# Optimization experiments

Measured on AMD Instinct MI355X. Metric: run time of the kernel, lower is better.

## Reference

```python
import jax, jax.numpy as jnp
import numpy as np

N = 2_000_000
N_IN = 128
N_HID = 32
CT_SIZE = 16384  # n_bags(1024) * n_ct(16)
N_CT = 16


def setup_inputs() -> dict:
    key = jax.random.key(0)
    ks = jax.random.split(key, 10)
    X = jax.random.normal(ks[0], (N, N_IN), dtype=jnp.float32)
    batch = jax.random.randint(ks[1], (N,), 0, CT_SIZE, dtype=jnp.int32)
    s = 1.0 / np.sqrt(N_IN)
    W1 = jax.random.uniform(ks[2], (N_IN, N_HID), jnp.float32, -s, s)
    b1 = jax.random.uniform(ks[3], (N_HID,), jnp.float32, -s, s)
    s2 = 1.0 / np.sqrt(N_HID)
    wc = jax.random.uniform(ks[4], (N_HID, 1), jnp.float32, -s2, s2)
    bc = jax.random.uniform(ks[5], (1,), jnp.float32, -s2, s2)
    wct = jax.random.uniform(ks[6], (N_HID, 1), jnp.float32, -s2, s2)
    bct = jax.random.uniform(ks[7], (1,), jnp.float32, -s2, s2)
    Wout = jax.random.uniform(ks[8], (N_HID, 1), jnp.float32, -s2, s2)
    bout = jax.random.uniform(ks[9], (1,), jnp.float32, -s2, s2)
    return {"X": X, "W1": W1, "b1": b1, "wc": wc, "bc": bc,
            "wct": wct, "bct": bct, "Wout": Wout, "bout": bout,
            "batch": batch, "ct_size": CT_SIZE, "n_ct": N_CT}


def _segment_softmax(s, batch, num_segments):
    # numerically stable softmax within each segment
    m = jax.ops.segment_max(s, batch, num_segments=num_segments)
    e = jnp.exp(s - m[batch])
    denom = jax.ops.segment_sum(e, batch, num_segments=num_segments)
    return e / denom[batch]


def reference(X, W1, b1, wc, bc, wct, bct, Wout, bout, batch, ct_size, n_ct):
    # lin: Linear(n_in, n_hid) + ReLU (dropout=0 in eval)
    H = jax.nn.relu(X @ W1 + b1)                          # [N, n_hid]
    # attn1 with use_softmax: segment softmax over cells within each (bag, celltype) segment
    s = (H @ wc + bc)[:, 0]                               # [N]
    w_c = _segment_softmax(s, batch, ct_size)             # [N]
    # global_add_pool of attention-weighted features, reshape to [n_bags, n_ct, n_hid]
    P = jax.ops.segment_sum(H * w_c[:, None], batch, num_segments=ct_size)
    P = P.reshape(-1, n_ct, N_HID)                        # [B, n_ct, n_hid]
    # lin2 is empty (n_layers_lin2=0)
    # attn2: softmax over cell-type axis
    w_ct = jax.nn.softmax(P @ wct + bct, axis=1)          # [B, n_ct, 1]
    Xb = jnp.sum(P * w_ct, axis=1)                        # [B, n_hid]
    return Xb @ Wout + bout                               # [B, 1]
```

## Files before the change

### kernel.cpp

```cpp
#include <hip/hip_runtime.h>
#include <hip/hip_bf16.h>
#include <cmath>

#define NIN   128
#define NHID  32
#define CTS   16384
#define NCT   16
#define NBAGS (CTS / NCT)
#define CAP   256
#define NBLK  128
#define SEG_STRIDE 33

typedef __attribute__((ext_vector_type(8))) short bf16x8;
typedef __attribute__((ext_vector_type(4))) float f32x4;

__device__ inline ushort f2bf(float f) {
    uint x = __float_as_uint(f);
    uint r = (x + 0x7fffu + ((x >> 16) & 1u)) >> 16;
    return (ushort)r;
}
__device__ inline float bf2f(ushort b) { return __uint_as_float(((uint)b) << 16); }


__global__ __launch_bounds__(1024) void hist_kernel(
    const int* __restrict__ batch, uint* __restrict__ hist, int n, int chunk)
{
    __shared__ uint h[CTS];
    const int b = blockIdx.x;
    for (int i = threadIdx.x; i < CTS; i += 1024) h[i] = 0;
    __syncthreads();
    const int lo = b * chunk, hi = min(n, lo + chunk);
    for (int i = lo + threadIdx.x; i < hi; i += 1024)
        atomicAdd(&h[batch[i]], 1u);
    __syncthreads();
    uint* __restrict__ hb = hist + (size_t)b * CTS;
    for (int i = threadIdx.x; i < CTS; i += 1024) hb[i] = h[i];
}

__global__ __launch_bounds__(256) void prefix_kernel(
    uint* __restrict__ hist, int* __restrict__ cnt)
{
    const int s = blockIdx.x * 256 + threadIdx.x;
    if (s >= CTS) return;
    uint run = 0;
#pragma unroll 4
    for (int b = 0; b < NBLK; ++b) {
        const uint t = hist[(size_t)b * CTS + s];
        hist[(size_t)b * CTS + s] = run;
        run += t;
    }
    cnt[s * 16] = (int)run;
}

__global__ __launch_bounds__(1024) void place_kernel(
    const int* __restrict__ batch, const uint* __restrict__ hist,
    int* __restrict__ slots, int n, int chunk)
{
    __shared__ uint h[CTS];
    const int b = blockIdx.x;
    const uint* __restrict__ hb = hist + (size_t)b * CTS;
    for (int i = threadIdx.x; i < CTS; i += 1024) h[i] = hb[i];
    __syncthreads();
    const int lo = b * chunk, hi = min(n, lo + chunk);
    for (int i = lo + threadIdx.x; i < hi; i += 1024) {
        const int s = batch[i];
        const uint pos = atomicAdd(&h[s], 1u);
        if (pos < CAP) slots[(size_t)s * CAP + pos] = i;
    }
}

__global__ __launch_bounds__(256) void seg_kernel(
    const float* __restrict__ X,
    const float* __restrict__ W1,
    const float* __restrict__ b1,
    const float* __restrict__ wc,
    const float* __restrict__ bc,
    const int*   __restrict__ cnt,
    const int*   __restrict__ slots,
    float* __restrict__ P)
{
    __shared__ __align__(16) float w1s[NIN * NHID];

    const int tid = threadIdx.x;
    for (int i = tid; i < NIN * NHID / 4; i += 256)
        ((float4*)w1s)[i] = ((const float4*)W1)[i];
    __syncthreads();

    const int w    = tid >> 6;
    const int lane = tid & 63;
    const int g    = lane >> 4;
    const int c    = lane & 15;
    const int s    = blockIdx.x * 4 + w;
    const int m    = min(cnt[s * 16], CAP);

    bf16x8 Bh[4][2], Bl[4][2];
#pragma unroll
    for (int kc = 0; kc < 4; ++kc) {
#pragma unroll
        for (int nh = 0; nh < 2; ++nh) {
            union { bf16x8 v; ushort u[8]; } bh, bl;
#pragma unroll
            for (int e = 0; e < 8; ++e) {
                const float wv = w1s[(kc * 32 + g * 8 + e) * NHID + nh * 16 + c];
                const ushort h = f2bf(wv);
                bh.u[e] = h;
                bl.u[e] = f2bf(wv - bf2f(h));
            }
            Bh[kc][nh] = bh.v;
            Bl[kc][nh] = bl.v;
        }
    }

    const float b1c0 = b1[c], b1c1 = b1[c + 16];
    const float wc0  = wc[c], wc1  = wc[c + 16];
    const float bc0  = bc[0];

    float pacc0 = 0.f, pacc1 = 0.f, esum = 0.f;
    const int ntiles = (m + 15) >> 4;
    const size_t sbase = (size_t)s * CAP;

    auto slot_of = [&](int t) -> int {
        const int ti = t * 16 + c;
        return slots[sbase + min(ti, m - 1)];
    };

    auto compute_tile = [&](const float4* x, int t) {
        f32x4 acc0 = {0.f, 0.f, 0.f, 0.f};
        f32x4 acc1 = {0.f, 0.f, 0.f, 0.f};
#pragma unroll
        for (int kc = 0; kc < 4; ++kc) {
            const float xs[8] = {x[2*kc].x, x[2*kc].y, x[2*kc].z, x[2*kc].w,
                                 x[2*kc+1].x, x[2*kc+1].y, x[2*kc+1].z, x[2*kc+1].w};
            union { bf16x8 v; __hip_bfloat162 h2[4]; } ah;
#pragma unroll
            for (int e = 0; e < 4; ++e)
                ah.h2[e] = __float22bfloat162_rn(make_float2(xs[2*e], xs[2*e+1]));

            acc0 = __builtin_amdgcn_mfma_f32_16x16x32_bf16(ah.v, Bh[kc][0], acc0, 0, 0, 0);
            acc0 = __builtin_amdgcn_mfma_f32_16x16x32_bf16(ah.v, Bl[kc][0], acc0, 0, 0, 0);
            acc1 = __builtin_amdgcn_mfma_f32_16x16x32_bf16(ah.v, Bh[kc][1], acc1, 0, 0, 0);
            acc1 = __builtin_amdgcn_mfma_f32_16x16x32_bf16(ah.v, Bl[kc][1], acc1, 0, 0, 0);
        }
#pragma unroll
        for (int i = 0; i < 4; ++i) {
            const float h0 = fmaxf(acc0[i] + b1c0, 0.f);
            const float h1 = fmaxf(acc1[i] + b1c1, 0.f);
            float sp = h0 * wc0 + h1 * wc1;
            sp += __shfl_xor(sp, 1);
            sp += __shfl_xor(sp, 2);
            sp += __shfl_xor(sp, 4);
            sp += __shfl_xor(sp, 8);
            const int row = t * 16 + g * 4 + i;
            const float e = (row < m) ? expf(sp + bc0) : 0.f;
            pacc0 = fmaf(e, h0, pacc0);
            pacc1 = fmaf(e, h1, pacc1);
            esum += e;
        }
    };

    auto load_tile = [&](float4* x, int r) {
        const float4* __restrict__ xr = (const float4*)(X + (size_t)r * NIN);
#pragma unroll
        for (int kc = 0; kc < 4; ++kc) {
            x[2*kc]   = xr[kc * 8 + g * 2];
            x[2*kc+1] = xr[kc * 8 + g * 2 + 1];
        }
    };

    if (ntiles > 0) {
        float4 xa[8];
        load_tile(xa, slot_of(0));
        int rnext = (ntiles > 1) ? slot_of(1) : 0;

        for (int t = 0; t < ntiles; ++t) {
            float4 xb[8];
            const bool more = (t + 1) < ntiles;
            if (more) load_tile(xb, rnext);
            const int rnn = (t + 2 < ntiles) ? slot_of(t + 2) : 0;
            compute_tile(xa, t);
#pragma unroll
            for (int q = 0; q < 8; ++q) xa[q] = xb[q];
            rnext = rnn;
        }
    }

    pacc0 += __shfl_xor(pacc0, 16); pacc0 += __shfl_xor(pacc0, 32);
    pacc1 += __shfl_xor(pacc1, 16); pacc1 += __shfl_xor(pacc1, 32);
    esum  += __shfl_xor(esum, 16);  esum  += __shfl_xor(esum, 32);

    if (lane < 16) {
        const float inv = esum > 0.f ? 1.f / esum : 0.f;
        P[(size_t)s * NHID + c]      = pacc0 * inv;
        P[(size_t)s * NHID + 16 + c] = pacc1 * inv;
    }
}

__global__ __launch_bounds__(256) void bags_kernel(
    const float* __restrict__ P,
    const float* __restrict__ wct,
    const float* __restrict__ bct,
    const float* __restrict__ Wout,
    const float* __restrict__ bout,
    float* __restrict__ out)
{
    const int b = blockIdx.x * blockDim.x + threadIdx.x;
    if (b >= NBAGS) return;

    float logit[NCT], dout[NCT];
#pragma unroll
    for (int ct = 0; ct < NCT; ++ct) {
        const float* p = P + (size_t)(b * NCT + ct) * NHID;
        float t = 0.f, d = 0.f;
#pragma unroll
        for (int j = 0; j < NHID; ++j) {
            const float pj = p[j];
            t += pj * wct[j];
            d += pj * Wout[j];
        }
        logit[ct] = t + bct[0];
        dout[ct]  = d;
    }

    float mx = logit[0];
#pragma unroll
    for (int ct = 1; ct < NCT; ++ct) mx = fmaxf(mx, logit[ct]);
    float den = 0.f, accv = 0.f;
#pragma unroll
    for (int ct = 0; ct < NCT; ++ct) {
        const float e = expf(logit[ct] - mx);
        den += e;
        accv += e * dout[ct];
    }
    out[b] = accv / den + bout[0];
}


__global__ __launch_bounds__(256) void rows_kernel_atomic(
    const float* __restrict__ X, const float* __restrict__ W1,
    const float* __restrict__ b1, const float* __restrict__ wc,
    const float* __restrict__ bc, const int* __restrict__ batch,
    float* __restrict__ segacc, int n)
{
    const long long r0 = (long long)blockIdx.x * 256 + threadIdx.x;
    if (r0 >= n) return;
    const float4* xp = (const float4*)(X + (size_t)r0 * NIN);
    float acc[NHID];
#pragma unroll
    for (int j = 0; j < NHID; ++j) acc[j] = 0.f;
#pragma unroll 4
    for (int kc = 0; kc < NIN / 4; ++kc) {
        const float4 xv = xp[kc];
        const float xa[4] = {xv.x, xv.y, xv.z, xv.w};
#pragma unroll
        for (int kk = 0; kk < 4; ++kk) {
            const float* wrow = W1 + (kc * 4 + kk) * NHID;
            const float u = xa[kk];
#pragma unroll
            for (int j = 0; j < NHID; ++j) acc[j] = fmaf(u, wrow[j], acc[j]);
        }
    }
    float sc = bc[0];
#pragma unroll
    for (int j = 0; j < NHID; ++j) {
        const float h = fmaxf(acc[j] + b1[j], 0.f); acc[j] = h; sc += h * wc[j];
    }
    const float e = expf(sc);
    float* p = segacc + (size_t)batch[r0] * SEG_STRIDE;
#pragma unroll
    for (int j = 0; j < NHID; ++j) atomicAdd(p + j, e * acc[j]);
    atomicAdd(p + NHID, e);
}

__global__ __launch_bounds__(256) void bags_kernel_fb(
    const float* __restrict__ segacc, const float* __restrict__ wct,
    const float* __restrict__ bct, const float* __restrict__ Wout,
    const float* __restrict__ bout, float* __restrict__ out)
{
    const int b = blockIdx.x * blockDim.x + threadIdx.x;
    if (b >= NBAGS) return;
    float logit[NCT], dout[NCT];
#pragma unroll
    for (int ct = 0; ct < NCT; ++ct) {
        const float* p = segacc + (size_t)(b * NCT + ct) * SEG_STRIDE;
        const float den = p[NHID];
        const float inv = den > 0.f ? 1.f / den : 0.f;
        float t = 0.f, d = 0.f;
#pragma unroll
        for (int j = 0; j < NHID; ++j) { const float pj = p[j]*inv; t += pj*wct[j]; d += pj*Wout[j]; }
        logit[ct] = t + bct[0];
        dout[ct]  = d;
    }
    float mx = logit[0];
#pragma unroll
    for (int ct = 1; ct < NCT; ++ct) mx = fmaxf(mx, logit[ct]);
    float den = 0.f, accv = 0.f;
#pragma unroll
    for (int ct = 0; ct < NCT; ++ct) {
        const float e = expf(logit[ct] - mx);
        den += e; accv += e * dout[ct];
    }
    out[b] = accv / den + bout[0];
}


extern "C" void kernel_launch(void* const* d_in, const int* in_sizes, int n_in,
                              void* d_out, int out_size, void* d_ws, size_t ws_size,
                              hipStream_t stream)
{
    const float* X    = (const float*)d_in[0];
    const float* W1   = (const float*)d_in[1];
    const float* b1   = (const float*)d_in[2];
    const float* wc   = (const float*)d_in[3];
    const float* bc   = (const float*)d_in[4];
    const float* wct  = (const float*)d_in[5];
    const float* bct  = (const float*)d_in[6];
    const float* Wout = (const float*)d_in[7];
    const float* bout = (const float*)d_in[8];
    const int*   batch= (const int*)d_in[9];
    const int n = in_sizes[9];

    const size_t cnt_bytes  = (size_t)CTS * 16 * sizeof(int);
    const size_t slot_bytes = (size_t)CTS * CAP * sizeof(int);
    const size_t p_bytes    = (size_t)CTS * NHID * sizeof(float);
    const size_t hist_bytes = (size_t)NBLK * CTS * sizeof(uint);
    const size_t need = cnt_bytes + slot_bytes + p_bytes + hist_bytes;

    if (ws_size >= need) {
        int*   cnt   = (int*)d_ws;
        int*   slots = cnt + (size_t)CTS * 16;
        float* P     = (float*)(slots + (size_t)CTS * CAP);
        uint*  hist  = (uint*)(P + (size_t)CTS * NHID);

        const int chunk = (n + NBLK - 1) / NBLK;
        hist_kernel<<<NBLK, 1024, 0, stream>>>(batch, hist, n, chunk);
        prefix_kernel<<<CTS / 256, 256, 0, stream>>>(hist, cnt);
        place_kernel<<<NBLK, 1024, 0, stream>>>(batch, hist, slots, n, chunk);
        seg_kernel<<<CTS / 4, 256, 0, stream>>>(X, W1, b1, wc, bc, cnt, slots, P);
        bags_kernel<<<(NBAGS + 255) / 256, 256, 0, stream>>>(
            P, wct, bct, Wout, bout, (float*)d_out);
    } else {
        float* segacc = (float*)d_ws;
        hipMemsetAsync(segacc, 0, (size_t)CTS * SEG_STRIDE * sizeof(float), stream);
        rows_kernel_atomic<<<(n + 255) / 256, 256, 0, stream>>>(
            X, W1, b1, wc, bc, batch, segacc, n);
        bags_kernel_fb<<<(NBAGS + 255) / 256, 256, 0, stream>>>(
            segacc, wct, bct, Wout, bout, (float*)d_out);
    }
}
```

Baseline: 310.1 us.

## Process three segments per wave with interleaved tile loads; double histogram blocks

Each wave in the segment kernel now handles three segments, round-robin interleaving their tiles so the X-row loads for one segment overlap the MFMA compute of the others. The goal is more memory-level parallelism and amortising the per-block W1 split-bf16 setup over more segments. Separately, the histogram and placement kernels use twice as many blocks. In exchange, register pressure rises from the three tile buffers and the grid gets fewer blocks, which may lower occupancy. The histogram workspace also doubles.

```diff
diff --git a/kernel.cpp b/kernel.cpp
--- a/kernel.cpp
+++ b/kernel.cpp
@@ -8,7 +8,7 @@
 #define NCT   16
 #define NBAGS (CTS / NCT)
 #define CAP   256
-#define NBLK  128
+#define NBLK  256
 #define SEG_STRIDE 33
 
 typedef __attribute__((ext_vector_type(8))) short bf16x8;
@@ -90,8 +90,6 @@
     const int lane = tid & 63;
     const int g    = lane >> 4;
     const int c    = lane & 15;
-    const int s    = blockIdx.x * 4 + w;
-    const int m    = min(cnt[s * 16], CAP);
 
     bf16x8 Bh[4][2], Bl[4][2];
 #pragma unroll
@@ -115,16 +113,33 @@
     const float wc0  = wc[c], wc1  = wc[c + 16];
     const float bc0  = bc[0];
 
-    float pacc0 = 0.f, pacc1 = 0.f, esum = 0.f;
-    const int ntiles = (m + 15) >> 4;
-    const size_t sbase = (size_t)s * CAP;
-
-    auto slot_of = [&](int t) -> int {
-        const int ti = t * 16 + c;
-        return slots[sbase + min(ti, m - 1)];
+    const int sBase = blockIdx.x * 12 + w * 3;
+    const int s0 = sBase, s1 = sBase + 1, s2 = sBase + 2;
+    const bool v0 = s0 < CTS, v1 = s1 < CTS, v2 = s2 < CTS;
+    const int m0 = v0 ? min(cnt[s0 * 16], CAP) : 0;
+    const int m1 = v1 ? min(cnt[s1 * 16], CAP) : 0;
+    const int m2 = v2 ? min(cnt[s2 * 16], CAP) : 0;
+    const int n0 = (m0 + 15) >> 4, n1 = (m1 + 15) >> 4, n2 = (m2 + 15) >> 4;
+
+    float pa00 = 0.f, pa01 = 0.f, es0 = 0.f;
+    float pa10 = 0.f, pa11 = 0.f, es1 = 0.f;
+    float pa20 = 0.f, pa21 = 0.f, es2 = 0.f;
+
+    auto slot_of = [&](int s, int m, int t) -> int {
+        return slots[(size_t)s * CAP + min(t * 16 + c, m - 1)];
     };
 
-    auto compute_tile = [&](const float4* x, int t) {
+    auto load_tile = [&](float4* x, int r) {
+        const float4* __restrict__ xr = (const float4*)(X + (size_t)r * NIN);
+#pragma unroll
+        for (int kc = 0; kc < 4; ++kc) {
+            x[2*kc]   = xr[kc * 8 + g * 2];
+            x[2*kc+1] = xr[kc * 8 + g * 2 + 1];
+        }
+    };
+
+    auto compute_tile = [&](const float4* x, int t, int m,
+                            float& pa0, float& pa1, float& es) {
         f32x4 acc0 = {0.f, 0.f, 0.f, 0.f};
         f32x4 acc1 = {0.f, 0.f, 0.f, 0.f};
 #pragma unroll
@@ -152,47 +167,51 @@
             sp += __shfl_xor(sp, 8);
             const int row = t * 16 + g * 4 + i;
             const float e = (row < m) ? expf(sp + bc0) : 0.f;
-            pacc0 = fmaf(e, h0, pacc0);
-            pacc1 = fmaf(e, h1, pacc1);
-            esum += e;
+            pa0 = fmaf(e, h0, pa0);
+            pa1 = fmaf(e, h1, pa1);
+            es += e;
         }
     };
 
-    auto load_tile = [&](float4* x, int r) {
-        const float4* __restrict__ xr = (const float4*)(X + (size_t)r * NIN);
-#pragma unroll
-        for (int kc = 0; kc < 4; ++kc) {
-            x[2*kc]   = xr[kc * 8 + g * 2];
-            x[2*kc+1] = xr[kc * 8 + g * 2 + 1];
+    float4 xa[8], xb[8], xc[8];
+    int t0 = 0, t1 = 0, t2 = 0;
+    int rn0 = 0, rn1 = 0, rn2 = 0;
+
+    if (n0 > 0) { load_tile(xa, slot_of(s0, m0, 0)); if (n0 > 1) rn0 = slot_of(s0, m0, 1); }
+    if (n1 > 0) { load_tile(xb, slot_of(s1, m1, 0)); if (n1 > 1) rn1 = slot_of(s1, m1, 1); }
+    if (n2 > 0) { load_tile(xc, slot_of(s2, m2, 0)); if (n2 > 1) rn2 = slot_of(s2, m2, 1); }
+
+    while (t0 < n0 || t1 < n1 || t2 < n2) {
+        if (t0 < n0) {
+            compute_tile(xa, t0, m0, pa00, pa01, es0);
+            ++t0;
+            if (t0 < n0) { load_tile(xa, rn0); if (t0 + 1 < n0) rn0 = slot_of(s0, m0, t0 + 1); }
+        }
+        if (t1 < n1) {
+            compute_tile(xb, t1, m1, pa10, pa11, es1);
+            ++t1;
+            if (t1 < n1) { load_tile(xb, rn1); if (t1 + 1 < n1) rn1 = slot_of(s1, m1, t1 + 1); }
+        }
+        if (t2 < n2) {
+            compute_tile(xc, t2, m2, pa20, pa21, es2);
+            ++t2;
+            if (t2 < n2) { load_tile(xc, rn2); if (t2 + 1 < n2) rn2 = slot_of(s2, m2, t2 + 1); }
+        }
+    }
+
+    auto finish = [&](int sQ, bool vQ, float pa0, float pa1, float es) {
+        pa0 += __shfl_xor(pa0, 16); pa0 += __shfl_xor(pa0, 32);
+        pa1 += __shfl_xor(pa1, 16); pa1 += __shfl_xor(pa1, 32);
+        es  += __shfl_xor(es, 16);  es  += __shfl_xor(es, 32);
+        if (vQ && lane < 16) {
+            const float inv = es > 0.f ? 1.f / es : 0.f;
+            P[(size_t)sQ * NHID + c]      = pa0 * inv;
+            P[(size_t)sQ * NHID + 16 + c] = pa1 * inv;
         }
     };
-
-    if (ntiles > 0) {
-        float4 xa[8];
-        load_tile(xa, slot_of(0));
-        int rnext = (ntiles > 1) ? slot_of(1) : 0;
-
-        for (int t = 0; t < ntiles; ++t) {
-            float4 xb[8];
-            const bool more = (t + 1) < ntiles;
-            if (more) load_tile(xb, rnext);
-            const int rnn = (t + 2 < ntiles) ? slot_of(t + 2) : 0;
-            compute_tile(xa, t);
-#pragma unroll
-            for (int q = 0; q < 8; ++q) xa[q] = xb[q];
-            rnext = rnn;
-        }
-    }
-
-    pacc0 += __shfl_xor(pacc0, 16); pacc0 += __shfl_xor(pacc0, 32);
-    pacc1 += __shfl_xor(pacc1, 16); pacc1 += __shfl_xor(pacc1, 32);
-    esum  += __shfl_xor(esum, 16);  esum  += __shfl_xor(esum, 32);
-
-    if (lane < 16) {
-        const float inv = esum > 0.f ? 1.f / esum : 0.f;
-        P[(size_t)s * NHID + c]      = pacc0 * inv;
-        P[(size_t)s * NHID + 16 + c] = pacc1 * inv;
-    }
+    finish(s0, v0, pa00, pa01, es0);
+    finish(s1, v1, pa10, pa11, es1);
+    finish(s2, v2, pa20, pa21, es2);
 }
 
 __global__ __launch_bounds__(256) void bags_kernel(
@@ -335,7 +354,8 @@
         hist_kernel<<<NBLK, 1024, 0, stream>>>(batch, hist, n, chunk);
         prefix_kernel<<<CTS / 256, 256, 0, stream>>>(hist, cnt);
         place_kernel<<<NBLK, 1024, 0, stream>>>(batch, hist, slots, n, chunk);
-        seg_kernel<<<CTS / 4, 256, 0, stream>>>(X, W1, b1, wc, bc, cnt, slots, P);
+        const int segBlocks = (CTS + 11) / 12;
+        seg_kernel<<<segBlocks, 256, 0, stream>>>(X, W1, b1, wc, bc, cnt, slots, P);
         bags_kernel<<<(NBAGS + 255) / 256, 256, 0, stream>>>(
             P, wct, bct, Wout, bout, (float*)d_out);
     } else {
```

Result: slower. 370.6 us (+19.5%).
